# Kernel tuning notes

Measured on AMD Instinct MI355X. Metric: run time of the kernel, lower is better.

## Reference

```python
import jax, jax.numpy as jnp
import numpy as np
import itertools

G = 80          # voxel grid side
N = 200000      # active voxels
A, B = 64, 128  # in/out channels
K = 27          # 3x3x3 kernel offsets
EPS = 1e-5


def _build_kernel_map():
    rng = np.random.default_rng(0)
    flat = rng.choice(G ** 3, size=N, replace=False)
    coords = np.stack(np.unravel_index(flat, (G, G, G)), axis=1).astype(np.int64)  # [N,3]
    lookup = np.full(G ** 3, -1, dtype=np.int64)
    lookup[flat] = np.arange(N)
    gidx = np.full((K, N), N, dtype=np.int32)  # pad with dummy row N
    sidx = np.full((K, N), N, dtype=np.int32)
    for k, off in enumerate(itertools.product([-1, 0, 1], repeat=3)):
        nb = coords + np.asarray(off)
        valid = np.all((nb >= 0) & (nb < G), axis=1)
        i_all = np.nonzero(valid)[0]
        nbf = np.ravel_multi_index(nb[valid].T, (G, G, G))
        j = lookup[nbf]
        m = j >= 0
        i, j = i_all[m], j[m]
        e = len(i)
        gidx[k, :e] = j   # gather neighbor features
        sidx[k, :e] = i   # scatter to output voxel
    return jnp.asarray(gidx), jnp.asarray(sidx)


def setup_inputs() -> dict:
    key = jax.random.key(0)
    ks = jax.random.split(key, 8)
    gidx, sidx = _build_kernel_map()
    return {
        "feats": jax.random.normal(ks[0], (N, A), jnp.float32),
        "w1": jax.random.normal(ks[1], (K, A, B), jnp.float32) * (1.0 / np.sqrt(K * A)),
        "w2": jax.random.normal(ks[2], (K, B, B), jnp.float32) * (1.0 / np.sqrt(K * B)),
        "w_nin": jax.random.normal(ks[3], (A, B), jnp.float32) * (1.0 / np.sqrt(A)),
        "bn1_gamma": jnp.ones((A,), jnp.float32),
        "bn1_beta": jnp.zeros((A,), jnp.float32),
        "bn2_gamma": jnp.ones((B,), jnp.float32),
        "bn2_beta": jnp.zeros((B,), jnp.float32),
        "gidx": gidx,
        "sidx": sidx,
    }


def _bn(x, gamma, beta):
    # MinkowskiBatchNorm: per-channel stats over all active voxels (training mode)
    mean = jnp.mean(x, axis=0)
    var = jnp.var(x, axis=0)
    return (x - mean) * jax.lax.rsqrt(var + EPS) * gamma + beta


def _sparse_conv(feats, w, gidx, sidx):
    # Minkowski sparse conv: for each kernel offset k, gather neighbor feats,
    # apply W[k], scatter-add to output voxel. Dummy row N absorbs padding.
    fp = jnp.concatenate([feats, jnp.zeros((1, feats.shape[1]), feats.dtype)], axis=0)
    out = jnp.zeros((N + 1, w.shape[-1]), feats.dtype)
    for k in range(w.shape[0]):  # fixed 27 offsets
        out = out.at[sidx[k]].add(fp[gidx[k]] @ w[k])
    return out[:N]


def reference(feats, w1, w2, w_nin, bn1_gamma, bn1_beta, bn2_gamma, bn2_beta, gidx, sidx):
    # resblock: BN(a) -> conv3(a->b) -> BN(b) -> conv3(b->b); skip via 1x1 conv (a!=b)
    h = _bn(feats, bn1_gamma, bn1_beta)
    h = _sparse_conv(h, w1, gidx, sidx)
    h = _bn(h, bn2_gamma, bn2_beta)
    residual = _sparse_conv(h, w2, gidx, sidx)
    skip = feats @ w_nin  # kernel_size=1 conv == per-voxel linear
    return skip + residual
```

## Files before the change

### kernel.cpp

```cpp
#include <hip/hip_runtime.h>

#define N_VOX 200000
#define NPAD_INV (27 * N_VOX + 128)
#define EPS_BN 1e-5f

typedef __bf16 bf16x8 __attribute__((ext_vector_type(8)));
typedef float f32x4 __attribute__((ext_vector_type(4)));

__device__ __forceinline__ float bf2f(unsigned short u) {
    union { float f; unsigned int i; } x; x.i = ((unsigned int)u) << 16; return x.f;
}
__device__ __forceinline__ unsigned short f2bf(float f) {
    union { float f; unsigned int i; } x; x.f = f;
    unsigned int r = x.i + 0x7fffu + ((x.i >> 16) & 1u);
    return (unsigned short)(r >> 16);
}

#define ASYNC16(gsrc, ldst)                                                             \
    __builtin_amdgcn_global_load_lds(                                                   \
        (const __attribute__((address_space(1))) void*)(gsrc),                          \
        (__attribute__((address_space(3))) void*)(ldst), 16, 0, 0)

__global__ void prep0_kernel(const float* __restrict__ feats, const float* __restrict__ w1,
                             const float* __restrict__ w2, const float* __restrict__ w_nin,
                             int* __restrict__ inv, unsigned short* __restrict__ w1t,
                             unsigned short* __restrict__ w2t, unsigned short* __restrict__ w_nint,
                             unsigned short* __restrict__ fRaw,
                             float* __restrict__ s1sum, float* __restrict__ s1sq) {
    __shared__ float rs[64], rq[64];
    const int t = threadIdx.x;
    if (t < 64) { rs[t] = 0.f; rq[t] = 0.f; }
    __syncthreads();
    const int stride = gridDim.x * 256;
    const int gid = blockIdx.x * 256 + t;
    for (int i = gid; i < NPAD_INV; i += stride) inv[i] = N_VOX;
    for (int i = gid; i < 8192; i += stride) {
        int a = i >> 7, b = i & 127;
        w_nint[b * 64 + a] = f2bf(w_nin[i]);
    }
    for (int e = gid; e < 27 * 8192; e += stride) {
        int k = e >> 13, idx = e & 8191;
        int a = idx >> 7, b = idx & 127;
        w1t[k * 8192 + b * 64 + a] = f2bf(w1[e]);
    }
    for (int e = gid; e < 27 * 16384; e += stride) {
        int k = e >> 14, idx = e & 16383;
        int a = idx >> 7, b = idx & 127;
        w2t[k * 16384 + b * 128 + a] = f2bf(w2[e]);
    }
    float s[8] = {}, q[8] = {};
    const int total = N_VOX * 64 / 8;
    for (int i = gid; i < total; i += stride) {
        const float4* src = (const float4*)(feats + (size_t)i * 8);
        float4 f0 = src[0], f1 = src[1];
        float fv[8] = {f0.x, f0.y, f0.z, f0.w, f1.x, f1.y, f1.z, f1.w};
        union { uint4 u4; unsigned short u[8]; } r;
#pragma unroll
        for (int j = 0; j < 8; j++) {
            r.u[j] = f2bf(fv[j]);
            s[j] += fv[j]; q[j] += fv[j] * fv[j];
        }
        *(uint4*)(fRaw + (size_t)i * 8) = r.u4;
    }
#pragma unroll
    for (int j = 0; j < 8; j++) {
        s[j] += __shfl_xor(s[j], 8, 64); s[j] += __shfl_xor(s[j], 16, 64); s[j] += __shfl_xor(s[j], 32, 64);
        q[j] += __shfl_xor(q[j], 8, 64); q[j] += __shfl_xor(q[j], 16, 64); q[j] += __shfl_xor(q[j], 32, 64);
    }
    const int lane = t & 63;
    if (lane < 8) {
#pragma unroll
        for (int j = 0; j < 8; j++) {
            atomicAdd(&rs[lane * 8 + j], s[j]);
            atomicAdd(&rq[lane * 8 + j], q[j]);
        }
    }
    __syncthreads();
    if (t < 64) { atomicAdd(&s1sum[t], rs[t]); atomicAdd(&s1sq[t], rq[t]); }
}

__global__ void prepbn_kernel(const int* __restrict__ sidx, const int* __restrict__ gidx,
                              int* __restrict__ inv, const unsigned short* __restrict__ fRaw,
                              const float* __restrict__ s1sum, const float* __restrict__ s1sq,
                              const float* __restrict__ g1, const float* __restrict__ b1,
                              unsigned short* __restrict__ fA) {
    __shared__ float sc[64], sh[64];
    const int t = threadIdx.x;
    if (t < 64) {
        float mean = s1sum[t] * (1.0f / N_VOX);
        float var  = s1sq[t] * (1.0f / N_VOX) - mean * mean;
        float s    = g1[t] * rsqrtf(var + EPS_BN);
        sc[t] = s; sh[t] = b1[t] - mean * s;
    }
    __syncthreads();
    const int stride = gridDim.x * 256;
    const int gid = blockIdx.x * 256 + t;
    for (int k = 0; k < 27; k++)
        for (int p = gid; p < N_VOX; p += stride) {
            int s = sidx[k * N_VOX + p];
            if (s < N_VOX) inv[k * N_VOX + s] = gidx[k * N_VOX + p];
        }
    const int total = N_VOX * 64 / 8;
    for (int i = gid; i < total; i += stride) {
        int cb = (i * 8) & 63;
        union { uint4 q; unsigned short u[8]; } v, a;
        v.q = *(const uint4*)(fRaw + (size_t)i * 8);
#pragma unroll
        for (int j = 0; j < 8; j++) a.u[j] = f2bf(bf2f(v.u[j]) * sc[cb + j] + sh[cb + j]);
        *(uint4*)(fA + (size_t)i * 8) = a.q;
    }
}

__global__ void stats2_kernel(const unsigned short* __restrict__ h1b,
                              float* __restrict__ sum, float* __restrict__ sq) {
    int t = threadIdx.x; int c = t & 127; int rg = t >> 7;
    float s = 0.f, q = 0.f;
    for (int row = blockIdx.x * 2 + rg; row < N_VOX; row += gridDim.x * 2) {
        float x = bf2f(h1b[(size_t)row * 128 + c]);
        s += x; q += x * x;
    }
    __shared__ float red[4][128];
    red[rg][c] = s; red[2 + rg][c] = q;
    __syncthreads();
    if (t < 128) atomicAdd(&sum[t], red[0][t] + red[1][t]);
    else { int cc = t - 128; atomicAdd(&sq[cc], red[2][cc] + red[3][cc]); }
}

__global__ void norm2_kernel(unsigned short* __restrict__ h1b, const float* __restrict__ ssum,
                             const float* __restrict__ ssq, const float* __restrict__ gamma,
                             const float* __restrict__ beta) {
    __shared__ float sc[128], sh[128];
    int t = threadIdx.x;
    if (t < 128) {
        float mean = ssum[t] * (1.0f / N_VOX);
        float var  = ssq[t] * (1.0f / N_VOX) - mean * mean;
        float s    = gamma[t] * rsqrtf(var + EPS_BN);
        sc[t] = s; sh[t] = beta[t] - mean * s;
    }
    __syncthreads();
    const int total = N_VOX * 128 / 8;
    int i = blockIdx.x * 256 + t;
    if (i >= total) return;
    int cb = (i * 8) & 127;
    union { uint4 q; unsigned short u[8]; } v;
    v.q = *(const uint4*)(h1b + (size_t)i * 8);
#pragma unroll
    for (int j = 0; j < 8; j++) v.u[j] = f2bf(bf2f(v.u[j]) * sc[cb + j] + sh[cb + j]);
    *(uint4*)(h1b + (size_t)i * 8) = v.q;
}

__global__ __launch_bounds__(256) void conv1_kernel(
    const unsigned short* __restrict__ fA, const unsigned short* __restrict__ w1t,
    const int* __restrict__ inv, const unsigned short* __restrict__ zp,
    unsigned short* __restrict__ h1b) {
    __shared__ __align__(16) unsigned short sA[2][128 * 64];
    __shared__ __align__(16) unsigned short sB[2][128 * 64];
    const int t = threadIdx.x, lane = t & 63, w = t >> 6;
    const int v0 = blockIdx.x * 128;
    const int srow = w * 32;
    const int lrow = lane >> 3;
    const int lcol = (lane & 7) * 8;
    const int scol = lcol ^ (lrow * 8);
    const int m0 = (w & 1) * 64, n0 = (w >> 1) * 64;
    const int l16 = lane & 15, quad = lane >> 4;
    const int xs = l16 & 7;
    f32x4 acc[4][4] = {};

    auto stage = [&](int k, int b) {
#pragma unroll
        for (int q = 0; q < 4; q++) {
            int rt = srow + q * 8 + lrow;
            int g = inv[k * N_VOX + v0 + rt];
            const unsigned short* asrc = (g < N_VOX) ? (fA + (size_t)g * 64 + scol) : (zp + scol);
            ASYNC16(asrc, &sA[b][(srow + q * 8) * 64]);
            const unsigned short* bsrc = w1t + k * 8192 + rt * 64 + scol;
            ASYNC16(bsrc, &sB[b][(srow + q * 8) * 64]);
        }
    };

    stage(0, 0);
    for (int j = 0; j < 27; j++) {
        const int cb = j & 1;
        if (j + 1 < 27) {
            stage(j + 1, cb ^ 1);
            asm volatile("s_waitcnt vmcnt(8)" ::: "memory");
        } else {
            asm volatile("s_waitcnt vmcnt(0)" ::: "memory");
        }
        __builtin_amdgcn_sched_barrier(0);
        __builtin_amdgcn_s_barrier();
        __builtin_amdgcn_sched_barrier(0);
#pragma unroll
        for (int ks = 0; ks < 2; ks++) {
            const int cs = ((ks * 4 + quad) ^ xs) * 8;
            bf16x8 af[4], bfr[4];
#pragma unroll
            for (int mi = 0; mi < 4; mi++)
                af[mi] = *(const bf16x8*)&sA[cb][(m0 + mi * 16 + l16) * 64 + cs];
#pragma unroll
            for (int ni = 0; ni < 4; ni++)
                bfr[ni] = *(const bf16x8*)&sB[cb][(n0 + ni * 16 + l16) * 64 + cs];
            __builtin_amdgcn_s_setprio(1);
#pragma unroll
            for (int mi = 0; mi < 4; mi++)
#pragma unroll
                for (int ni = 0; ni < 4; ni++)
                    acc[mi][ni] = __builtin_amdgcn_mfma_f32_16x16x32_bf16(af[mi], bfr[ni], acc[mi][ni], 0, 0, 0);
            __builtin_amdgcn_s_setprio(0);
        }
        __builtin_amdgcn_sched_barrier(0);
        __builtin_amdgcn_s_barrier();
        __builtin_amdgcn_sched_barrier(0);
    }
#pragma unroll
    for (int mi = 0; mi < 4; mi++)
#pragma unroll
        for (int r = 0; r < 4; r++) {
            int v = v0 + m0 + mi * 16 + quad * 4 + r;
            if (v < N_VOX) {
#pragma unroll
                for (int ni = 0; ni < 4; ni++)
                    h1b[(size_t)v * 128 + n0 + ni * 16 + l16] = f2bf(acc[mi][ni][r]);
            }
        }
}

__global__ __launch_bounds__(256) void conv2_kernel(
    const unsigned short* __restrict__ h1n, const unsigned short* __restrict__ fRaw,
    const unsigned short* __restrict__ w2t, const unsigned short* __restrict__ w_nint,
    const int* __restrict__ inv, const unsigned short* __restrict__ zp,
    float* __restrict__ out) {
    __shared__ __align__(16) unsigned short sA[2][128 * 64];
    __shared__ __align__(16) unsigned short sB[2][128 * 64];
    const int t = threadIdx.x, lane = t & 63, w = t >> 6;
    const int v0 = blockIdx.x * 128;
    const int srow = w * 32;
    const int lrow = lane >> 3;
    const int lcol = (lane & 7) * 8;
    const int scol = lcol ^ (lrow * 8);
    const int m0 = (w & 1) * 64, n0 = (w >> 1) * 64;
    const int l16 = lane & 15, quad = lane >> 4;
    const int xs = l16 & 7;
    f32x4 acc[4][4] = {};

    auto stage = [&](int j, int b) {
        if (j < 54) {
            const int ko = j >> 1;
            const int kh = (j & 1) * 64;
#pragma unroll
            for (int q = 0; q < 4; q++) {
                int rt = srow + q * 8 + lrow;
                int g = inv[ko * N_VOX + v0 + rt];
                const unsigned short* asrc = (g < N_VOX) ? (h1n + (size_t)g * 128 + kh + scol) : (zp + scol);
                ASYNC16(asrc, &sA[b][(srow + q * 8) * 64]);
                const unsigned short* bsrc = w2t + ko * 16384 + rt * 128 + kh + scol;
                ASYNC16(bsrc, &sB[b][(srow + q * 8) * 64]);
            }
        } else {
#pragma unroll
            for (int q = 0; q < 4; q++) {
                int rt = srow + q * 8 + lrow;
                int v = v0 + rt;
                const unsigned short* asrc = (v < N_VOX) ? (fRaw + (size_t)v * 64 + scol) : (zp + scol);
                ASYNC16(asrc, &sA[b][(srow + q * 8) * 64]);
                const unsigned short* bsrc = w_nint + rt * 64 + scol;
                ASYNC16(bsrc, &sB[b][(srow + q * 8) * 64]);
            }
        }
    };

    stage(0, 0);
    for (int jj = 0; jj < 55; jj++) {
        const int cb = jj & 1;
        if (jj + 1 < 55) {
            stage(jj + 1, cb ^ 1);
            asm volatile("s_waitcnt vmcnt(8)" ::: "memory");
        } else {
            asm volatile("s_waitcnt vmcnt(0)" ::: "memory");
        }
        __builtin_amdgcn_sched_barrier(0);
        __builtin_amdgcn_s_barrier();
        __builtin_amdgcn_sched_barrier(0);
#pragma unroll
        for (int ks = 0; ks < 2; ks++) {
            const int cs = ((ks * 4 + quad) ^ xs) * 8;
            bf16x8 af[4], bfr[4];
#pragma unroll
            for (int mi = 0; mi < 4; mi++)
                af[mi] = *(const bf16x8*)&sA[cb][(m0 + mi * 16 + l16) * 64 + cs];
#pragma unroll
            for (int ni = 0; ni < 4; ni++)
                bfr[ni] = *(const bf16x8*)&sB[cb][(n0 + ni * 16 + l16) * 64 + cs];
            __builtin_amdgcn_s_setprio(1);
#pragma unroll
            for (int mi = 0; mi < 4; mi++)
#pragma unroll
                for (int ni = 0; ni < 4; ni++)
                    acc[mi][ni] = __builtin_amdgcn_mfma_f32_16x16x32_bf16(af[mi], bfr[ni], acc[mi][ni], 0, 0, 0);
            __builtin_amdgcn_s_setprio(0);
        }
        __builtin_amdgcn_sched_barrier(0);
        __builtin_amdgcn_s_barrier();
        __builtin_amdgcn_sched_barrier(0);
    }
#pragma unroll
    for (int mi = 0; mi < 4; mi++)
#pragma unroll
        for (int r = 0; r < 4; r++) {
            int v = v0 + m0 + mi * 16 + quad * 4 + r;
            if (v < N_VOX) {
#pragma unroll
                for (int ni = 0; ni < 4; ni++)
                    out[(size_t)v * 128 + n0 + ni * 16 + l16] = acc[mi][ni][r];
            }
        }
}

extern "C" void kernel_launch(void* const* d_in, const int* in_sizes, int n_in,
                              void* d_out, int out_size, void* d_ws, size_t ws_size,
                              hipStream_t stream) {
    const float* feats = (const float*)d_in[0];
    const float* w1    = (const float*)d_in[1];
    const float* w2    = (const float*)d_in[2];
    const float* w_nin = (const float*)d_in[3];
    const float* g1    = (const float*)d_in[4];
    const float* b1    = (const float*)d_in[5];
    const float* g2    = (const float*)d_in[6];
    const float* b2    = (const float*)d_in[7];
    const int* gidx = (const int*)d_in[8];
    const int* sidx = (const int*)d_in[9];
    float* out = (float*)d_out;

    char* ws = (char*)d_ws;
    int* inv               = (int*)(ws);
    unsigned short* fRaw   = (unsigned short*)(ws + 21600512);
    unsigned short* fA     = (unsigned short*)(ws + 47200512);
    unsigned short* h1b    = (unsigned short*)(ws + 72800512);
    unsigned short* w1t    = (unsigned short*)(ws + 124000512);
    unsigned short* w2t    = (unsigned short*)(ws + 124442880);
    unsigned short* w_nint = (unsigned short*)(ws + 125327616);
    float* stats           = (float*)(ws + 125344000);
    unsigned short* zp     = (unsigned short*)(ws + 125345536);
    float* s1sum = stats, *s1sq = stats + 64, *s2sum = stats + 128, *s2sq = stats + 256;

    hipMemsetAsync(stats, 0, 1536 + 256, stream);
    prep0_kernel<<<1024, 256, 0, stream>>>(feats, w1, w2, w_nin, inv, w1t, w2t, w_nint,
                                           fRaw, s1sum, s1sq);
    prepbn_kernel<<<1024, 256, 0, stream>>>(sidx, gidx, inv, fRaw, s1sum, s1sq, g1, b1, fA);
    conv1_kernel<<<1563, 256, 0, stream>>>(fA, w1t, inv, zp, h1b);
    stats2_kernel<<<512, 256, 0, stream>>>(h1b, s2sum, s2sq);
    norm2_kernel<<<12500, 256, 0, stream>>>(h1b, s2sum, s2sq, g2, b2);
    conv2_kernel<<<1563, 256, 0, stream>>>(h1b, fRaw, w2t, w_nint, inv, zp, out);
}
```

Measured before the change: 745.9 us.

## Fuse BN2 statistics into conv1 epilogue and trim inverse-map build

Computes per-channel sum and sum-of-squares for the second batch norm inside the conv1 epilogue, using wave shuffles and shared-memory atomics, and removes the separate stats2 pass that re-read h1b. The prepbn kernel now binary-searches where each offset's padding starts, so it only scans the valid region of sidx when building the inverse map. The conv2 output stores become nontemporal. Statistics are now taken from the fp32 accumulators rather than the bf16-rounded values. Both the fusion and the binary search assume the padding in sidx is contiguous at the tail of each row.

```diff
diff --git a/kernel.cpp b/kernel.cpp
--- a/kernel.cpp
+++ b/kernel.cpp
@@ -85,6 +85,7 @@
                               const float* __restrict__ g1, const float* __restrict__ b1,
                               unsigned short* __restrict__ fA) {
     __shared__ float sc[64], sh[64];
+    __shared__ int ek[27];
     const int t = threadIdx.x;
     if (t < 64) {
         float mean = s1sum[t] * (1.0f / N_VOX);
@@ -92,14 +93,24 @@
         float s    = g1[t] * rsqrtf(var + EPS_BN);
         sc[t] = s; sh[t] = b1[t] - mean * s;
     }
+    if (t < 27) {
+        int lo = 0, hi = N_VOX;
+        while (lo < hi) {
+            int mid = (lo + hi) >> 1;
+            if (sidx[t * N_VOX + mid] == N_VOX) hi = mid; else lo = mid + 1;
+        }
+        ek[t] = lo;
+    }
     __syncthreads();
     const int stride = gridDim.x * 256;
     const int gid = blockIdx.x * 256 + t;
-    for (int k = 0; k < 27; k++)
-        for (int p = gid; p < N_VOX; p += stride) {
+    for (int k = 0; k < 27; k++) {
+        const int e = ek[k];
+        for (int p = gid; p < e; p += stride) {
             int s = sidx[k * N_VOX + p];
-            if (s < N_VOX) inv[k * N_VOX + s] = gidx[k * N_VOX + p];
-        }
+            inv[k * N_VOX + s] = gidx[k * N_VOX + p];
+        }
+    }
     const int total = N_VOX * 64 / 8;
     for (int i = gid; i < total; i += stride) {
         int cb = (i * 8) & 63;
@@ -109,21 +120,6 @@
         for (int j = 0; j < 8; j++) a.u[j] = f2bf(bf2f(v.u[j]) * sc[cb + j] + sh[cb + j]);
         *(uint4*)(fA + (size_t)i * 8) = a.q;
     }
-}
-
-__global__ void stats2_kernel(const unsigned short* __restrict__ h1b,
-                              float* __restrict__ sum, float* __restrict__ sq) {
-    int t = threadIdx.x; int c = t & 127; int rg = t >> 7;
-    float s = 0.f, q = 0.f;
-    for (int row = blockIdx.x * 2 + rg; row < N_VOX; row += gridDim.x * 2) {
-        float x = bf2f(h1b[(size_t)row * 128 + c]);
-        s += x; q += x * x;
-    }
-    __shared__ float red[4][128];
-    red[rg][c] = s; red[2 + rg][c] = q;
-    __syncthreads();
-    if (t < 128) atomicAdd(&sum[t], red[0][t] + red[1][t]);
-    else { int cc = t - 128; atomicAdd(&sq[cc], red[2][cc] + red[3][cc]); }
 }
 
 __global__ void norm2_kernel(unsigned short* __restrict__ h1b, const float* __restrict__ ssum,
@@ -152,9 +148,10 @@
 __global__ __launch_bounds__(256) void conv1_kernel(
     const unsigned short* __restrict__ fA, const unsigned short* __restrict__ w1t,
     const int* __restrict__ inv, const unsigned short* __restrict__ zp,
-    unsigned short* __restrict__ h1b) {
+    unsigned short* __restrict__ h1b, float* __restrict__ s2sum, float* __restrict__ s2sq) {
     __shared__ __align__(16) unsigned short sA[2][128 * 64];
     __shared__ __align__(16) unsigned short sB[2][128 * 64];
+    __shared__ float s2s[128], s2q[128];
     const int t = threadIdx.x, lane = t & 63, w = t >> 6;
     const int v0 = blockIdx.x * 128;
     const int srow = w * 32;
@@ -166,6 +163,8 @@
     const int xs = l16 & 7;
     f32x4 acc[4][4] = {};
 
+    if (t < 128) { s2s[t] = 0.f; s2q[t] = 0.f; }
+
     auto stage = [&](int k, int b) {
 #pragma unroll
         for (int q = 0; q < 4; q++) {
@@ -212,6 +211,8 @@
         __builtin_amdgcn_s_barrier();
         __builtin_amdgcn_sched_barrier(0);
     }
+
+    float ps[4] = {}, pq[4] = {};
 #pragma unroll
     for (int mi = 0; mi < 4; mi++)
 #pragma unroll
@@ -219,10 +220,27 @@
             int v = v0 + m0 + mi * 16 + quad * 4 + r;
             if (v < N_VOX) {
 #pragma unroll
-                for (int ni = 0; ni < 4; ni++)
-                    h1b[(size_t)v * 128 + n0 + ni * 16 + l16] = f2bf(acc[mi][ni][r]);
+                for (int ni = 0; ni < 4; ni++) {
+                    float x = acc[mi][ni][r];
+                    ps[ni] += x; pq[ni] += x * x;
+                    h1b[(size_t)v * 128 + n0 + ni * 16 + l16] = f2bf(x);
+                }
             }
         }
+#pragma unroll
+    for (int ni = 0; ni < 4; ni++) {
+        ps[ni] += __shfl_xor(ps[ni], 16, 64); ps[ni] += __shfl_xor(ps[ni], 32, 64);
+        pq[ni] += __shfl_xor(pq[ni], 16, 64); pq[ni] += __shfl_xor(pq[ni], 32, 64);
+    }
+    if (lane < 16) {
+#pragma unroll
+        for (int ni = 0; ni < 4; ni++) {
+            atomicAdd(&s2s[n0 + ni * 16 + lane], ps[ni]);
+            atomicAdd(&s2q[n0 + ni * 16 + lane], pq[ni]);
+        }
+    }
+    __syncthreads();
+    if (t < 128) { atomicAdd(&s2sum[t], s2s[t]); atomicAdd(&s2sq[t], s2q[t]); }
 }
 
 __global__ __launch_bounds__(256) void conv2_kernel(
@@ -311,7 +329,8 @@
             if (v < N_VOX) {
 #pragma unroll
                 for (int ni = 0; ni < 4; ni++)
-                    out[(size_t)v * 128 + n0 + ni * 16 + l16] = acc[mi][ni][r];
+                    __builtin_nontemporal_store(acc[mi][ni][r],
+                                                &out[(size_t)v * 128 + n0 + ni * 16 + l16]);
             }
         }
 }
@@ -347,8 +366,7 @@
     prep0_kernel<<<1024, 256, 0, stream>>>(feats, w1, w2, w_nin, inv, w1t, w2t, w_nint,
                                            fRaw, s1sum, s1sq);
     prepbn_kernel<<<1024, 256, 0, stream>>>(sidx, gidx, inv, fRaw, s1sum, s1sq, g1, b1, fA);
-    conv1_kernel<<<1563, 256, 0, stream>>>(fA, w1t, inv, zp, h1b);
-    stats2_kernel<<<512, 256, 0, stream>>>(h1b, s2sum, s2sq);
+    conv1_kernel<<<1563, 256, 0, stream>>>(fA, w1t, inv, zp, h1b, s2sum, s2sq);
     norm2_kernel<<<12500, 256, 0, stream>>>(h1b, s2sum, s2sq, g2, b2);
     conv2_kernel<<<1563, 256, 0, stream>>>(h1b, fRaw, w2t, w_nint, inv, zp, out);
 }
```

Result: faster. 701.4 us (-6.0%).
